# Performance work log

Measured on AMD Instinct MI355X. Metric: run time of the kernel, lower is better.

## Reference

```python
import jax, jax.numpy as jnp
import numpy as np

EMBED_DIM = 1024
N_HEADS = 16
HEAD_DIM = EMBED_DIM // N_HEADS
B, T = 4, 2048


def setup_inputs() -> dict:
    key = jax.random.key(0)
    ks = jax.random.split(key, 5)
    s = 1.0 / np.sqrt(EMBED_DIM)
    return {
        "x": jax.random.normal(ks[0], (B, T, EMBED_DIM), dtype=jnp.float32),
        "w_qkv": jax.random.normal(ks[1], (EMBED_DIM, 3 * EMBED_DIM), dtype=jnp.float32) * s,
        "b_qkv": jnp.zeros((3 * EMBED_DIM,), dtype=jnp.float32),
        "w_out": jax.random.normal(ks[2], (EMBED_DIM, EMBED_DIM), dtype=jnp.float32) * s,
        "b_out": jnp.zeros((EMBED_DIM,), dtype=jnp.float32),
    }


def reference(x, w_qkv, b_qkv, w_out, b_out):
    Bb, Tt, C = x.shape
    qkv = x @ w_qkv + b_qkv                      # (B, T, 3C)
    q, k, v = jnp.split(qkv, 3, axis=-1)
    # (B, H, T, Dh)
    def to_heads(t):
        return t.reshape(Bb, Tt, N_HEADS, HEAD_DIM).transpose(0, 2, 1, 3)
    q, k, v = to_heads(q), to_heads(k), to_heads(v)
    scale = 1.0 / np.sqrt(HEAD_DIM)
    scores = jnp.einsum("bhqd,bhkd->bhqk", q, k) * scale  # (B, H, T, T)
    causal = jnp.tril(jnp.ones((Tt, Tt), dtype=bool))
    scores = jnp.where(causal[None, None], scores, -jnp.inf)
    attn = jax.nn.softmax(scores, axis=-1)
    out = jnp.einsum("bhqk,bhkd->bhqd", attn, v)  # (B, H, T, Dh)
    out = out.transpose(0, 2, 1, 3).reshape(Bb, Tt, C)
    return out @ w_out + b_out
```

## Files before the change

kernel.cpp:

```cpp
#include <hip/hip_runtime.h>

typedef __bf16 bf16;
typedef __bf16 bf16x4 __attribute__((ext_vector_type(4)));
typedef __bf16 bf16x8 __attribute__((ext_vector_type(8)));
typedef float f32x4 __attribute__((ext_vector_type(4)));

#define TSEQ 2048
#define NHEAD 16

__device__ __forceinline__ void gload_lds16(const bf16* g, bf16* s) {
  __builtin_amdgcn_global_load_lds(
      (const __attribute__((address_space(1))) void*)g,
      (__attribute__((address_space(3))) void*)s, 16, 0, 0);
}

__global__ __launch_bounds__(256) void prep_kernel(
    const float* __restrict__ x, bf16* __restrict__ xbf,
    const float* __restrict__ w_qkv, bf16* __restrict__ wqkvt,
    const float* __restrict__ w_out, bf16* __restrict__ woutt) {
  __shared__ float tile[32][33];
  const int bid = blockIdx.x;
  const int tid = threadIdx.x;
  if (bid < 4096) {
    size_t i = ((size_t)bid * 256 + tid) * 8;
    float4 v0 = ((const float4*)(x + i))[0];
    float4 v1 = ((const float4*)(x + i))[1];
    bf16x8 o;
    o[0] = (bf16)v0.x; o[1] = (bf16)v0.y; o[2] = (bf16)v0.z; o[3] = (bf16)v0.w;
    o[4] = (bf16)v1.x; o[5] = (bf16)v1.y; o[6] = (bf16)v1.z; o[7] = (bf16)v1.w;
    *(bf16x8*)(xbf + i) = o;
    return;
  }
  const float* in; bf16* out; int K, N, n0, k0;
  if (bid < 7168) {
    int q = bid - 4096;
    in = w_qkv; out = wqkvt; K = 1024; N = 3072;
    n0 = (q % 96) * 32; k0 = (q / 96) * 32;
  } else {
    int q = bid - 7168;
    in = w_out; out = woutt; K = 1024; N = 1024;
    n0 = (q & 31) * 32; k0 = (q >> 5) * 32;
  }
  int tx = tid & 31, ty = tid >> 5;
#pragma unroll
  for (int i = ty; i < 32; i += 8)
    tile[i][tx] = in[(size_t)(k0 + i) * N + n0 + tx];
  __syncthreads();
#pragma unroll
  for (int i = ty; i < 32; i += 8)
    out[(size_t)(n0 + i) * K + k0 + tx] = (bf16)tile[tx][i];
}

template <typename OutT>
__global__ __launch_bounds__(256, 4) void gemm_bf16_kernel(
    const bf16* __restrict__ A, const bf16* __restrict__ Bt,
    const float* __restrict__ bias, OutT* __restrict__ C,
    int M, int N, int K, int scale_cols, bf16* __restrict__ vp) {
  alignas(16) __shared__ bf16 As[128 * 64];
  alignas(16) __shared__ bf16 Bs[128 * 64];
  const int row0 = blockIdx.y * 128, col0 = blockIdx.x * 128;
  const int tid = threadIdx.x;
  const int wave = tid >> 6, lane = tid & 63;
  const int quad = lane >> 4, lm = lane & 15;
  const int wm = (wave >> 1) * 64, wn = (wave & 1) * 64;

  f32x4 acc[4][4];
  const f32x4 z4 = {0.0f, 0.0f, 0.0f, 0.0f};
#pragma unroll
  for (int i = 0; i < 4; i++)
#pragma unroll
    for (int j = 0; j < 4; j++) acc[i][j] = z4;

  const int sr0 = tid >> 3;
  const int js = (tid & 7) ^ ((tid >> 4) & 7);
  const bf16* apg = A + (size_t)(row0 + sr0) * K + js * 8;
  const bf16* bpg = Bt + (size_t)(col0 + sr0) * K + js * 8;
  const size_t row32 = (size_t)32 * K;

  const int sw = (lm >> 1) & 7;

  for (int k0 = 0; k0 < K; k0 += 64) {
    __syncthreads();
#pragma unroll
    for (int p = 0; p < 4; p++) {
      gload_lds16(apg + p * row32, &As[(p * 256 + tid) * 8]);
      gload_lds16(bpg + p * row32, &Bs[(p * 256 + tid) * 8]);
    }
    apg += 64; bpg += 64;
    __syncthreads();

#pragma unroll
    for (int ks = 0; ks < 2; ks++) {
      const int kc = ((ks * 4 + quad) ^ sw) * 8;
      bf16x8 af[4], bfr[4];
#pragma unroll
      for (int i = 0; i < 4; i++)
        af[i] = *(const bf16x8*)&As[(wm + i * 16 + lm) * 64 + kc];
#pragma unroll
      for (int j = 0; j < 4; j++)
        bfr[j] = *(const bf16x8*)&Bs[(wn + j * 16 + lm) * 64 + kc];
#pragma unroll
      for (int i = 0; i < 4; i++)
#pragma unroll
        for (int j = 0; j < 4; j++)
          acc[i][j] = __builtin_amdgcn_mfma_f32_16x16x32_bf16(af[i], bfr[j], acc[i][j], 0, 0, 0);
    }
  }

#pragma unroll
  for (int j = 0; j < 4; j++) {
    int gc = col0 + wn + j * 16 + lm;
    float bb = bias[gc];
    float sc2 = (gc < scale_cols) ? 0.125f : 1.0f;
    if (vp != nullptr && gc >= 2048) {
      int gr0 = row0 + wm + quad * 4;
      int b = gr0 >> 11;
      size_t vrow = (size_t)(b * 1024 + gc - 2048) * TSEQ;
#pragma unroll
      for (int i = 0; i < 4; i++) {
        int t = (gr0 + i * 16) & (TSEQ - 1);
        bf16x4 vk;
#pragma unroll
        for (int rr = 0; rr < 4; rr++) vk[rr] = (bf16)(acc[i][j][rr] + bb);
        *(bf16x4*)(vp + vrow + t) = vk;
      }
    } else {
#pragma unroll
      for (int i = 0; i < 4; i++) {
        int gr = row0 + wm + i * 16 + quad * 4;
#pragma unroll
        for (int rr = 0; rr < 4; rr++) {
          float v = (acc[i][j][rr] + bb) * sc2;
          C[(size_t)(gr + rr) * N + gc] = (OutT)v;
        }
      }
    }
  }
}

__global__ __launch_bounds__(256, 4) void flash_attn_kernel(
    const bf16* __restrict__ qkv, const bf16* __restrict__ vp,
    bf16* __restrict__ att) {
  alignas(16) __shared__ bf16 Ks[64 * 64];
  alignas(16) __shared__ bf16 Vts[64 * 64];
  alignas(16) __shared__ bf16 Ps[4][32 * 64];

  const int hb = blockIdx.x;
  const int h = hb & 15, b = hb >> 4;
  const int y = blockIdx.y;
  const int g = y >> 2, r = y & 3;
  const int qt = (g == 0) ? (15 - r) : (g == 1) ? r : (g == 2) ? (11 - r) : (4 + r);
  const int q0 = qt * 128;
  const int tid = threadIdx.x;
  const int wave = tid >> 6, lane = tid & 63;
  const int quad = lane >> 4, lm = lane & 15;
  const size_t rowbase = (size_t)b * TSEQ;
  const f32x4 z4 = {0.0f, 0.0f, 0.0f, 0.0f};

  bf16x8 bq[2][2];
#pragma unroll
  for (int nf = 0; nf < 2; nf++)
#pragma unroll
    for (int ks = 0; ks < 2; ks++)
      bq[nf][ks] = *(const bf16x8*)(qkv +
          (rowbase + q0 + wave * 32 + nf * 16 + lm) * 3072 + h * 64 + ks * 32 + quad * 8);

  const int strow = tid >> 3;
  const int js = (tid & 7) ^ ((tid >> 4) & 7);
  const bf16* kstg = qkv + (rowbase + strow) * 3072 + 1024 + h * 64 + js * 8;
  const bf16* vstg = vp + ((size_t)hb * 64 + strow) * TSEQ + js * 8;
  const size_t krow32 = (size_t)32 * 3072;
  const size_t vrow32 = (size_t)32 * TSEQ;

  const int sw = (lm >> 1) & 7;

  f32x4 oT[4][2];
#pragma unroll
  for (int mf = 0; mf < 4; mf++)
#pragma unroll
    for (int nf = 0; nf < 2; nf++) oT[mf][nf] = z4;
  float lp[2] = {0.0f, 0.0f};

  const int nkt = 2 * qt + 2;
  const int wrow_lo = q0 + wave * 32;
  const int wrow_hi = wrow_lo + 31;

  for (int kt = 0; kt < nkt; kt++) {
    const int k0 = kt * 64;
    __syncthreads();
    gload_lds16(kstg + (size_t)k0 * 3072, &Ks[tid * 8]);
    gload_lds16(kstg + (size_t)k0 * 3072 + krow32, &Ks[(256 + tid) * 8]);
    gload_lds16(vstg + k0, &Vts[tid * 8]);
    gload_lds16(vstg + k0 + vrow32, &Vts[(256 + tid) * 8]);
    __syncthreads();
    if (k0 > wrow_hi) continue;

    f32x4 s[4][2];
#pragma unroll
    for (int mf = 0; mf < 4; mf++)
#pragma unroll
      for (int nf = 0; nf < 2; nf++) s[mf][nf] = z4;
#pragma unroll
    for (int ks = 0; ks < 2; ks++) {
      const int kc = ((ks * 4 + quad) ^ sw) * 8;
      bf16x8 ak[4];
#pragma unroll
      for (int mf = 0; mf < 4; mf++)
        ak[mf] = *(const bf16x8*)&Ks[(mf * 16 + lm) * 64 + kc];
#pragma unroll
      for (int mf = 0; mf < 4; mf++)
#pragma unroll
        for (int nf = 0; nf < 2; nf++)
          s[mf][nf] = __builtin_amdgcn_mfma_f32_16x16x32_bf16(ak[mf], bq[nf][ks], s[mf][nf], 0, 0, 0);
    }

    const bool need_mask = (k0 + 63 > wrow_lo);
#pragma unroll
    for (int nf = 0; nf < 2; nf++) {
      const int qrow = q0 + wave * 32 + nf * 16 + lm;
#pragma unroll
      for (int mf = 0; mf < 4; mf++) {
        bf16x4 pk;
        float psum = 0.0f;
#pragma unroll
        for (int rr = 0; rr < 4; rr++) {
          float pv = __expf(s[mf][nf][rr]);
          if (need_mask) {
            int kv = k0 + mf * 16 + quad * 4 + rr;
            pv = (kv > qrow) ? 0.0f : pv;
          }
          psum += pv;
          pk[rr] = (bf16)pv;
        }
        lp[nf] += psum;
        *(bf16x4*)&Ps[wave][(nf * 16 + lm) * 64 +
                            (((mf * 2 + (quad >> 1)) ^ sw) * 8 + (quad & 1) * 4)] = pk;
      }
    }

#pragma unroll
    for (int ks = 0; ks < 2; ks++) {
      const int kc = ((ks * 4 + quad) ^ sw) * 8;
      bf16x8 av[4], bp[2];
#pragma unroll
      for (int mf = 0; mf < 4; mf++)
        av[mf] = *(const bf16x8*)&Vts[(mf * 16 + lm) * 64 + kc];
#pragma unroll
      for (int nf = 0; nf < 2; nf++)
        bp[nf] = *(const bf16x8*)&Ps[wave][(nf * 16 + lm) * 64 + kc];
#pragma unroll
      for (int mf = 0; mf < 4; mf++)
#pragma unroll
        for (int nf = 0; nf < 2; nf++)
          oT[mf][nf] = __builtin_amdgcn_mfma_f32_16x16x32_bf16(av[mf], bp[nf], oT[mf][nf], 0, 0, 0);
    }
  }

  float linv[2];
#pragma unroll
  for (int nf = 0; nf < 2; nf++) {
    float l = lp[nf];
    l += __shfl_xor(l, 16, 64);
    l += __shfl_xor(l, 32, 64);
    linv[nf] = 1.0f / l;
  }

#pragma unroll
  for (int nf = 0; nf < 2; nf++) {
    const size_t grow = rowbase + q0 + wave * 32 + nf * 16 + lm;
#pragma unroll
    for (int mf = 0; mf < 4; mf++) {
      bf16x4 ok;
#pragma unroll
      for (int rr = 0; rr < 4; rr++) ok[rr] = (bf16)(oT[mf][nf][rr] * linv[nf]);
      *(bf16x4*)(att + grow * 1024 + h * 64 + mf * 16 + quad * 4) = ok;
    }
  }
}

extern "C" void kernel_launch(void* const* d_in, const int* in_sizes, int n_in,
                              void* d_out, int out_size, void* d_ws, size_t ws_size,
                              hipStream_t stream) {
  const float* x = (const float*)d_in[0];
  const float* w_qkv = (const float*)d_in[1];
  const float* b_qkv = (const float*)d_in[2];
  const float* w_out = (const float*)d_in[3];
  const float* b_out = (const float*)d_in[4];
  float* out = (float*)d_out;

  char* ws = (char*)d_ws;
  bf16* Xbf   = (bf16*)(ws);
  bf16* Wqkvt = (bf16*)(ws + 16777216);
  bf16* Woutt = (bf16*)(ws + 23068672);
  bf16* QKV   = (bf16*)(ws + 25165824);
  bf16* VP    = (bf16*)(ws + 75497472);
  bf16* ATT   = (bf16*)(ws + 92274688);

  prep_kernel<<<8192, 256, 0, stream>>>(x, Xbf, w_qkv, Wqkvt, w_out, Woutt);
  gemm_bf16_kernel<bf16><<<dim3(24, 64), 256, 0, stream>>>(
      Xbf, Wqkvt, b_qkv, QKV, 8192, 3072, 1024, 1024, VP);
  flash_attn_kernel<<<dim3(64, 16, 1), 256, 0, stream>>>(QKV, VP, ATT);
  gemm_bf16_kernel<float><<<dim3(8, 64), 256, 0, stream>>>(
      ATT, Woutt, b_out, out, 8192, 1024, 1024, 0, nullptr);
}
```

Baseline: 245.0 us.

## Fold log2e into Q scale, compact QK buffer, narrow out-proj tile

Folds log2(e) into the query scale so the softmax can use a native exp2 instruction instead of __expf. The QKV buffer is shrunk to hold only Q and K (ldc 2048), since V is already written transposed to its own buffer. This cuts workspace size and makes K loads strided over 2048 instead of 3072. The output projection GEMM now uses a 64-wide N tile, which doubles the block count from 512 to 1024 for better CU occupancy, and ATT reuses the Xbf workspace region.

```diff
diff --git a/kernel.cpp b/kernel.cpp
--- a/kernel.cpp
+++ b/kernel.cpp
@@ -7,6 +7,14 @@
 
 #define TSEQ 2048
 #define NHEAD 16
+
+#define QSCALE 0.18033688011112042f
+
+#if __has_builtin(__builtin_amdgcn_exp2f)
+#define EXP2F(x) __builtin_amdgcn_exp2f(x)
+#else
+#define EXP2F(x) exp2f(x)
+#endif
 
 __device__ __forceinline__ void gload_lds16(const bf16* g, bf16* s) {
   __builtin_amdgcn_global_load_lds(
@@ -51,25 +59,28 @@
     out[(size_t)(n0 + i) * K + k0 + tx] = (bf16)tile[tx][i];
 }
 
-template <typename OutT>
+template <typename OutT, int BN>
 __global__ __launch_bounds__(256, 4) void gemm_bf16_kernel(
     const bf16* __restrict__ A, const bf16* __restrict__ Bt,
     const float* __restrict__ bias, OutT* __restrict__ C,
-    int M, int N, int K, int scale_cols, bf16* __restrict__ vp) {
+    int M, int N, int K, int ldc, float scale0, int scale_cols,
+    bf16* __restrict__ vp) {
+  constexpr int BG = BN / 32;
+  constexpr int JN = BN / 32;
   alignas(16) __shared__ bf16 As[128 * 64];
-  alignas(16) __shared__ bf16 Bs[128 * 64];
-  const int row0 = blockIdx.y * 128, col0 = blockIdx.x * 128;
+  alignas(16) __shared__ bf16 Bs[BN * 64];
+  const int row0 = blockIdx.y * 128, col0 = blockIdx.x * BN;
   const int tid = threadIdx.x;
   const int wave = tid >> 6, lane = tid & 63;
   const int quad = lane >> 4, lm = lane & 15;
-  const int wm = (wave >> 1) * 64, wn = (wave & 1) * 64;
-
-  f32x4 acc[4][4];
+  const int wm = (wave >> 1) * 64, wn = (wave & 1) * (BN / 2);
+
+  f32x4 acc[4][JN];
   const f32x4 z4 = {0.0f, 0.0f, 0.0f, 0.0f};
 #pragma unroll
   for (int i = 0; i < 4; i++)
 #pragma unroll
-    for (int j = 0; j < 4; j++) acc[i][j] = z4;
+    for (int j = 0; j < JN; j++) acc[i][j] = z4;
 
   const int sr0 = tid >> 3;
   const int js = (tid & 7) ^ ((tid >> 4) & 7);
@@ -82,36 +93,37 @@
   for (int k0 = 0; k0 < K; k0 += 64) {
     __syncthreads();
 #pragma unroll
-    for (int p = 0; p < 4; p++) {
+    for (int p = 0; p < 4; p++)
       gload_lds16(apg + p * row32, &As[(p * 256 + tid) * 8]);
+#pragma unroll
+    for (int p = 0; p < BG; p++)
       gload_lds16(bpg + p * row32, &Bs[(p * 256 + tid) * 8]);
-    }
     apg += 64; bpg += 64;
     __syncthreads();
 
 #pragma unroll
     for (int ks = 0; ks < 2; ks++) {
       const int kc = ((ks * 4 + quad) ^ sw) * 8;
-      bf16x8 af[4], bfr[4];
+      bf16x8 af[4], bfr[JN];
 #pragma unroll
       for (int i = 0; i < 4; i++)
         af[i] = *(const bf16x8*)&As[(wm + i * 16 + lm) * 64 + kc];
 #pragma unroll
-      for (int j = 0; j < 4; j++)
+      for (int j = 0; j < JN; j++)
         bfr[j] = *(const bf16x8*)&Bs[(wn + j * 16 + lm) * 64 + kc];
 #pragma unroll
       for (int i = 0; i < 4; i++)
 #pragma unroll
-        for (int j = 0; j < 4; j++)
+        for (int j = 0; j < JN; j++)
           acc[i][j] = __builtin_amdgcn_mfma_f32_16x16x32_bf16(af[i], bfr[j], acc[i][j], 0, 0, 0);
     }
   }
 
 #pragma unroll
-  for (int j = 0; j < 4; j++) {
+  for (int j = 0; j < JN; j++) {
     int gc = col0 + wn + j * 16 + lm;
     float bb = bias[gc];
-    float sc2 = (gc < scale_cols) ? 0.125f : 1.0f;
+    float sc2 = (gc < scale_cols) ? scale0 : 1.0f;
     if (vp != nullptr && gc >= 2048) {
       int gr0 = row0 + wm + quad * 4;
       int b = gr0 >> 11;
@@ -131,7 +143,7 @@
 #pragma unroll
         for (int rr = 0; rr < 4; rr++) {
           float v = (acc[i][j][rr] + bb) * sc2;
-          C[(size_t)(gr + rr) * N + gc] = (OutT)v;
+          C[(size_t)(gr + rr) * ldc + gc] = (OutT)v;
         }
       }
     }
@@ -139,7 +151,7 @@
 }
 
 __global__ __launch_bounds__(256, 4) void flash_attn_kernel(
-    const bf16* __restrict__ qkv, const bf16* __restrict__ vp,
+    const bf16* __restrict__ qk, const bf16* __restrict__ vp,
     bf16* __restrict__ att) {
   alignas(16) __shared__ bf16 Ks[64 * 64];
   alignas(16) __shared__ bf16 Vts[64 * 64];
@@ -162,14 +174,14 @@
   for (int nf = 0; nf < 2; nf++)
 #pragma unroll
     for (int ks = 0; ks < 2; ks++)
-      bq[nf][ks] = *(const bf16x8*)(qkv +
-          (rowbase + q0 + wave * 32 + nf * 16 + lm) * 3072 + h * 64 + ks * 32 + quad * 8);
+      bq[nf][ks] = *(const bf16x8*)(qk +
+          (rowbase + q0 + wave * 32 + nf * 16 + lm) * 2048 + h * 64 + ks * 32 + quad * 8);
 
   const int strow = tid >> 3;
   const int js = (tid & 7) ^ ((tid >> 4) & 7);
-  const bf16* kstg = qkv + (rowbase + strow) * 3072 + 1024 + h * 64 + js * 8;
+  const bf16* kstg = qk + (rowbase + strow) * 2048 + 1024 + h * 64 + js * 8;
   const bf16* vstg = vp + ((size_t)hb * 64 + strow) * TSEQ + js * 8;
-  const size_t krow32 = (size_t)32 * 3072;
+  const size_t krow32 = (size_t)32 * 2048;
   const size_t vrow32 = (size_t)32 * TSEQ;
 
   const int sw = (lm >> 1) & 7;
@@ -188,8 +200,8 @@
   for (int kt = 0; kt < nkt; kt++) {
     const int k0 = kt * 64;
     __syncthreads();
-    gload_lds16(kstg + (size_t)k0 * 3072, &Ks[tid * 8]);
-    gload_lds16(kstg + (size_t)k0 * 3072 + krow32, &Ks[(256 + tid) * 8]);
+    gload_lds16(kstg + (size_t)k0 * 2048, &Ks[tid * 8]);
+    gload_lds16(kstg + (size_t)k0 * 2048 + krow32, &Ks[(256 + tid) * 8]);
     gload_lds16(vstg + k0, &Vts[tid * 8]);
     gload_lds16(vstg + k0 + vrow32, &Vts[(256 + tid) * 8]);
     __syncthreads();
@@ -224,7 +236,7 @@
         float psum = 0.0f;
 #pragma unroll
         for (int rr = 0; rr < 4; rr++) {
-          float pv = __expf(s[mf][nf][rr]);
+          float pv = EXP2F(s[mf][nf][rr]);
           if (need_mask) {
             int kv = k0 + mf * 16 + quad * 4 + rr;
             pv = (kv > qrow) ? 0.0f : pv;
@@ -290,16 +302,16 @@
 
   char* ws = (char*)d_ws;
   bf16* Xbf   = (bf16*)(ws);
+  bf16* ATT   = (bf16*)(ws);
   bf16* Wqkvt = (bf16*)(ws + 16777216);
   bf16* Woutt = (bf16*)(ws + 23068672);
-  bf16* QKV   = (bf16*)(ws + 25165824);
-  bf16* VP    = (bf16*)(ws + 75497472);
-  bf16* ATT   = (bf16*)(ws + 92274688);
+  bf16* QK    = (bf16*)(ws + 25165824);
+  bf16* VP    = (bf16*)(ws + 58720256);
 
   prep_kernel<<<8192, 256, 0, stream>>>(x, Xbf, w_qkv, Wqkvt, w_out, Woutt);
-  gemm_bf16_kernel<bf16><<<dim3(24, 64), 256, 0, stream>>>(
-      Xbf, Wqkvt, b_qkv, QKV, 8192, 3072, 1024, 1024, VP);
-  flash_attn_kernel<<<dim3(64, 16, 1), 256, 0, stream>>>(QKV, VP, ATT);
-  gemm_bf16_kernel<float><<<dim3(8, 64), 256, 0, stream>>>(
-      ATT, Woutt, b_out, out, 8192, 1024, 1024, 0, nullptr);
-}
+  gemm_bf16_kernel<bf16, 128><<<dim3(24, 64), 256, 0, stream>>>(
+      Xbf, Wqkvt, b_qkv, QK, 8192, 3072, 1024, 2048, QSCALE, 1024, VP);
+  flash_attn_kernel<<<dim3(64, 16, 1), 256, 0, stream>>>(QK, VP, ATT);
+  gemm_bf16_kernel<float, 64><<<dim3(16, 64), 256, 0, stream>>>(
+      ATT, Woutt, b_out, out, 8192, 1024, 1024, 1024, 1.0f, 0, nullptr);
+}
```

Result: no change. 240.9 us (-1.7%).
